# Kernel optimization log

Hardware: AMD Instinct MI355X
Metric: run time of the kernel (lower is better)

Reference implementation:

```python
import jax, jax.numpy as jnp
import numpy as np

B, Cin, Cout, H, W = 8, 64, 128, 128, 128
K, S, P = 3, 1, 1
KK = K * K
EPS = 1e-5


def _conv2d(x, w, b=None):
    out = jax.lax.conv_general_dilated(
        x, w, window_strides=(S, S), padding=[(P, P), (P, P)],
        dimension_numbers=('NCHW', 'OIHW', 'NCHW'))
    if b is not None:
        out = out + b[None, :, None, None]
    return out


def setup_inputs() -> dict:
    key = jax.random.key(0)
    k = jax.random.split(key, 5)
    sc = 1.0 / np.sqrt(Cin * KK)
    return {
        'x': jax.random.normal(k[0], (B, Cin, H, W), jnp.float32),
        'offset_w': jax.random.normal(k[1], (2 * KK, Cin, K, K), jnp.float32) * sc,
        'offset_b': jnp.zeros((2 * KK,), jnp.float32),
        'mask_w': jax.random.normal(k[2], (KK, Cin, K, K), jnp.float32) * sc,
        'mask_b': jnp.zeros((KK,), jnp.float32),
        'conv_w': jax.random.normal(k[3], (Cout, Cin, K, K), jnp.float32) * sc,
    }


def _deform_conv2d(x, offset, mask, w):
    """Modulated deformable conv (torchvision deform_conv2d semantics)."""
    Bn, C, Hh, Ww = x.shape
    Ho, Wo = offset.shape[2], offset.shape[3]
    off = offset.reshape(Bn, KK, 2, Ho, Wo)  # (y, x) pairs per kernel tap
    ky, kx = jnp.meshgrid(jnp.arange(K), jnp.arange(K), indexing='ij')
    ky = ky.reshape(KK).astype(x.dtype)
    kx = kx.reshape(KK).astype(x.dtype)
    hy = (jnp.arange(Ho) * S - P).astype(x.dtype)
    wx = (jnp.arange(Wo) * S - P).astype(x.dtype)
    # sampling positions [B, KK, Ho, Wo]
    py = off[:, :, 0] + ky[None, :, None, None] + hy[None, None, :, None]
    px = off[:, :, 1] + kx[None, :, None, None] + wx[None, None, None, :]

    y0 = jnp.floor(py)
    x0 = jnp.floor(px)
    wy1 = py - y0; wx1 = px - x0
    wy0 = 1.0 - wy1; wx0 = 1.0 - wx1

    xf = x.reshape(Bn, C, Hh * Ww)

    def gather(yi, xi):
        valid = ((yi >= 0) & (yi < Hh) & (xi >= 0) & (xi < Ww)).astype(x.dtype)
        yc = jnp.clip(yi, 0, Hh - 1).astype(jnp.int32)
        xc = jnp.clip(xi, 0, Ww - 1).astype(jnp.int32)
        idx = (yc * Ww + xc).reshape(Bn, -1)  # [B, KK*Ho*Wo]
        vals = jnp.take_along_axis(xf, idx[:, None, :], axis=2)  # [B, C, KK*Ho*Wo]
        return vals.reshape(Bn, C, KK, Ho, Wo) * valid.reshape(Bn, 1, KK, Ho, Wo)

    v = (gather(y0, x0) * (wy0 * wx0)[:, None]
         + gather(y0, x0 + 1) * (wy0 * wx1)[:, None]
         + gather(y0 + 1, x0) * (wy1 * wx0)[:, None]
         + gather(y0 + 1, x0 + 1) * (wy1 * wx1)[:, None])  # [B, C, KK, Ho, Wo]
    v = v * mask[:, None]  # modulation
    return jnp.einsum('bckhw,ock->bohw', v, w.reshape(w.shape[0], C, KK))


def reference(x, offset_w, offset_b, mask_w, mask_b, conv_w):
    offset = _conv2d(x, offset_w, offset_b)
    mask = jax.nn.sigmoid(_conv2d(x, mask_w, mask_b))
    out = _deform_conv2d(x, offset, mask, conv_w)
    # BatchNorm2d(affine=False), training-mode normalization over (N, H, W)
    mean = out.mean(axis=(0, 2, 3), keepdims=True)
    var = out.var(axis=(0, 2, 3), keepdims=True)
    return jax.nn.relu((out - mean) * jax.lax.rsqrt(var + EPS))
```

## Files before the change

kernel.cpp:

```cpp
#include <hip/hip_runtime.h>
#include <hip/hip_bf16.h>

#define H_ 128
#define W_ 128
#define HW 16384
#define CIN 64
#define COUT 128
#define KK9 9
#define BATCH 8
#define NPIX (BATCH * HW)
#define KDIM 576

typedef short bf16x8 __attribute__((ext_vector_type(8)));
typedef float f32x4  __attribute__((ext_vector_type(4)));
typedef unsigned short ushort_t;

union U4B { uint4 u; bf16x8 v; };

__device__ __forceinline__ float us2f(unsigned short u) {
    unsigned int v = ((unsigned int)u) << 16;
    float f;
    __builtin_memcpy(&f, &v, 4);
    return f;
}
__device__ __forceinline__ float lo_f(unsigned int w) {
    unsigned int v = w << 16;
    float f;
    __builtin_memcpy(&f, &v, 4);
    return f;
}
__device__ __forceinline__ float hi_f(unsigned int w) {
    unsigned int v = w & 0xffff0000u;
    float f;
    __builtin_memcpy(&f, &v, 4);
    return f;
}
__device__ __forceinline__ unsigned short f2us_bf(float f) {
    __hip_bfloat16 h = __float2bfloat16(f);
    unsigned short u;
    __builtin_memcpy(&u, &h, 2);
    return u;
}
__device__ __forceinline__ unsigned int pack2(float a, float b) {
    return (unsigned int)f2us_bf(a) | ((unsigned int)f2us_bf(b) << 16);
}

template <bool F32>
__device__ __forceinline__ float ld_in(const void* p, long i) {
    if (F32) return ((const float*)p)[i];
    return us2f(((const unsigned short*)p)[i]);
}

__global__ void detect_zero(const uint4* __restrict__ xr4,
                            float* __restrict__ flag,
                            float* __restrict__ gstat) {
    int t = threadIdx.x;
#pragma unroll
    for (int i = 0; i < 16; ++i) gstat[i * 256 + t] = 0.0f;
    if (t < 64) {
        uint4 v = xr4[t];
        unsigned int w[4] = {v.x, v.y, v.z, v.w};
        int big = 0;
#pragma unroll
        for (int q = 0; q < 4; ++q) {
            big += (((w[q] >> 7)  & 0xFF) >= 0xC0);
            big += (((w[q] >> 23) & 0xFF) >= 0xC0);
        }
        unsigned long long m = __ballot(big > 0);
        if (t == 0) flag[0] = m ? 1.0f : 0.0f;
    }
}

template <bool F32>
__device__ __forceinline__ void prep_body(const void* offw, const void* offb,
                                          const void* maskw, const void* maskb,
                                          const void* convw,
                                          ushort_t* wTs, ushort_t* wcats,
                                          float* bias, int i) {
    if (i < 73728) {
        int j = i & 7, lane = (i >> 3) & 63, n = (i >> 9) & 7, ks = i >> 12;
        int co = n * 16 + (lane & 15);
        int k  = ks * 32 + ((lane >> 4) << 3) + j;
        int kk = k >> 6, ci = k & 63;
        wTs[i] = f2us_bf(ld_in<F32>(convw, (long)co * KDIM + ci * 9 + kk));
    } else if (i < 73728 + 18432) {
        int i2 = i - 73728;
        int j = i2 & 7, lane = (i2 >> 3) & 63, n = (i2 >> 9) & 1, ks = i2 >> 10;
        int co2 = n * 16 + (lane & 15);
        int k   = ks * 32 + ((lane >> 4) << 3) + j;
        int kk = k >> 6, ci = k & 63;
        float v = 0.0f;
        if (co2 < 18)      v = ld_in<F32>(offw,  (long)co2 * KDIM + ci * 9 + kk);
        else if (co2 < 27) v = ld_in<F32>(maskw, (long)(co2 - 18) * KDIM + ci * 9 + kk);
        wcats[i2] = f2us_bf(v);
    } else if (i < 73728 + 18432 + 32) {
        int j = i - 73728 - 18432;
        float v = 0.0f;
        if (j < 18)      v = ld_in<F32>(offb, j);
        else if (j < 27) v = ld_in<F32>(maskb, j - 18);
        bias[j] = v;
    }
}

__global__ void prep_weights(const void* __restrict__ offw,
                             const void* __restrict__ offb,
                             const void* __restrict__ maskw,
                             const void* __restrict__ maskb,
                             const void* __restrict__ convw,
                             const float* __restrict__ flag,
                             ushort_t* __restrict__ wTs,
                             ushort_t* __restrict__ wcats,
                             float* __restrict__ bias) {
    int i = blockIdx.x * 256 + threadIdx.x;
    if (flag[0] != 0.0f)
        prep_body<true>(offw, offb, maskw, maskb, convw, wTs, wcats, bias, i);
    else
        prep_body<false>(offw, offb, maskw, maskb, convw, wTs, wcats, bias, i);
}

template <bool F32>
__device__ __forceinline__ void transpose_body(const void* x, ushort_t* xnb) {
    __shared__ float tile[CIN][64 + 1];
    int blk  = blockIdx.x;
    int b    = blk >> 8;
    int pix0 = (blk & 255) * 64;
    int t    = threadIdx.x;
    int lane = t & 63;
    int grp  = t >> 6;
#pragma unroll
    for (int r = 0; r < 16; ++r) {
        int ci = r * 4 + grp;
        tile[ci][lane] = ld_in<F32>(x, (long)(b * CIN + ci) * HW + pix0 + lane);
    }
    __syncthreads();
#pragma unroll
    for (int r = 0; r < 16; ++r) {
        int px = r * 4 + grp;
        xnb[(size_t)(b * HW + pix0 + px) * CIN + lane] = f2us_bf(tile[lane][px]);
    }
}

__global__ __launch_bounds__(256) void transpose_x(const void* __restrict__ x,
                                                   const float* __restrict__ flag,
                                                   ushort_t* __restrict__ xnb) {
    if (flag[0] != 0.0f) transpose_body<true>(x, xnb);
    else                 transpose_body<false>(x, xnb);
}

__global__ __launch_bounds__(1024, 4) void conv_mfma(
        const ushort_t* __restrict__ xnb,
        const ushort_t* __restrict__ wcats,
        const float* __restrict__ bias,
        float* __restrict__ off2,
        float* __restrict__ mask_ws) {
    __shared__ uint4 ldsB4[2304];
    __shared__ uint4 ldsX4[4096];

    int t    = threadIdx.x;
    int bid  = blockIdx.x;
    int sbid = (bid & 7) * 64 + (bid >> 3);
    int pix0 = sbid * 256;
    int b    = pix0 >> 14;
    int rem0 = pix0 & 16383;
    int y0   = rem0 >> 7;

    const uint4* ws4 = (const uint4*)wcats;
#pragma unroll
    for (int i = t; i < 2304; i += 1024) ldsB4[i] = ws4[i];

    const uint4* xrow4 = (const uint4*)(xnb + (size_t)b * HW * CIN);
    int sxq  = t >> 3;
    int sc16 = t & 7;
#pragma unroll
    for (int r = 0; r < 4; ++r) {
        int gy = y0 - 1 + r;
        if (gy >= 0 && gy < H_) {
            uint4 v = xrow4[(size_t)gy * 1024 + t];
            ldsX4[r * 1024 + sxq * 8 + (sc16 ^ (sxq & 7))] = v;
        }
    }
    __syncthreads();

    int wave = t >> 6, lane = t & 63, mrow = lane & 15, quad = lane >> 4;
    int px_l = wave * 16 + mrow;
    int ly   = px_l >> 7;
    int xp   = px_l & 127;

    uint4 af0[9], af1[9];
#pragma unroll
    for (int kk = 0; kk < 9; ++kk) {
        int ty = kk / 3, tx = kk % 3;
        int tr = ly + ty;
        int gy = y0 - 1 + tr;
        int xq = xp + tx - 1;
        bool ok = (gy >= 0) && (gy < H_) && (xq >= 0) && (xq < W_);
        int xc = min(max(xq, 0), W_ - 1);
        int base = tr * 1024 + xc * 8;
        uint4 a0 = ldsX4[base + ((quad    ) ^ (xc & 7))];
        uint4 a1 = ldsX4[base + ((quad + 4) ^ (xc & 7))];
        af0[kk] = ok ? a0 : make_uint4(0, 0, 0, 0);
        af1[kk] = ok ? a1 : make_uint4(0, 0, 0, 0);
    }

    f32x4 acc[2];
    acc[0] = (f32x4){0.f, 0.f, 0.f, 0.f};
    acc[1] = (f32x4){0.f, 0.f, 0.f, 0.f};
    const ushort_t* ldsB = (const ushort_t*)ldsB4;
#pragma unroll
    for (int kk = 0; kk < 9; ++kk) {
#pragma unroll
        for (int half = 0; half < 2; ++half) {
            int ks = kk * 2 + half;
            U4B a; a.u = half ? af1[kk] : af0[kk];
#pragma unroll
            for (int n = 0; n < 2; ++n) {
                bf16x8 bf = *(const bf16x8*)(ldsB + ((ks * 2 + n) * 64 + lane) * 8);
                acc[n] = __builtin_amdgcn_mfma_f32_16x16x32_bf16(a.v, bf, acc[n], 0, 0, 0);
            }
        }
    }

#pragma unroll
    for (int n = 0; n < 2; ++n) {
        int co2 = n * 16 + mrow;
        if (co2 >= 27) continue;
        float bs = bias[co2];
#pragma unroll
        for (int r = 0; r < 4; ++r) {
            int px = wave * 16 + quad * 4 + r;
            float v = acc[n][r] + bs;
            if (co2 < 18) {
                off2[((size_t)(b * 9 + (co2 >> 1)) * HW + rem0 + px) * 2 + (co2 & 1)] = v;
            } else {
                mask_ws[(size_t)(b * 9 + (co2 - 18)) * HW + rem0 + px] =
                    1.0f / (1.0f + __expf(-v));
            }
        }
    }
}

__device__ __forceinline__ void compute_tap(int yp_t, int xp_t,
                                            float oy, float ox, float mk,
                                            int* ofs, float* wg) {
    float py  = (float)yp_t + oy;
    float pxf = (float)xp_t + ox;
    float y0f = floorf(py), x0f = floorf(pxf);
    int yi = (int)y0f, xi = (int)x0f;
    float wy1 = py - y0f, wx1 = pxf - x0f;
    float wy0 = 1.0f - wy1, wx0 = 1.0f - wx1;
    int ya  = min(max(yi, 0), H_ - 1);
    int yb  = min(max(yi + 1, 0), H_ - 1);
    int xa  = min(max(xi, 0), W_ - 1);
    int xb2 = min(max(xi + 1, 0), W_ - 1);
    bool vy0 = (yi >= 0) & (yi < H_);
    bool vy1 = (yi >= -1) & (yi < H_ - 1);
    bool vx0 = (xi >= 0) & (xi < W_);
    bool vx1 = (xi >= -1) & (xi < W_ - 1);
    float m0 = mk * wy0, m1 = mk * wy1;
    wg[0] = (vy0 & vx0) ? m0 * wx0 : 0.0f;
    wg[1] = (vy0 & vx1) ? m0 * wx1 : 0.0f;
    wg[2] = (vy1 & vx0) ? m1 * wx0 : 0.0f;
    wg[3] = (vy1 & vx1) ? m1 * wx1 : 0.0f;
    int ra = ya << 13, rb = yb << 13;
    int ca = xa << 6,  cb_ = xb2 << 6;
    ofs[0] = ra + ca;  ofs[1] = ra + cb_;
    ofs[2] = rb + ca;  ofs[3] = rb + cb_;
}

__device__ __forceinline__ void issue_half(const ushort_t* __restrict__ xb,
                                           const int* ofs, int hoff, uint4* cb) {
#pragma unroll
    for (int c = 0; c < 4; ++c)
        cb[c] = *(const uint4*)(xb + ofs[c] + hoff);
}

__device__ __forceinline__ void consume_half(int ks, const uint4* cb,
                                             const float* wg,
                                             const ushort_t* __restrict__ ldsB,
                                             int lane, f32x4* acc) {
    float2 v2[4];
#pragma unroll
    for (int j = 0; j < 4; ++j) v2[j] = make_float2(0.f, 0.f);
#pragma unroll
    for (int c = 0; c < 4; ++c) {
        float w = wg[c];
        unsigned int ww[4] = {cb[c].x, cb[c].y, cb[c].z, cb[c].w};
#pragma unroll
        for (int j = 0; j < 4; ++j) {
            v2[j].x = fmaf(w, lo_f(ww[j]), v2[j].x);
            v2[j].y = fmaf(w, hi_f(ww[j]), v2[j].y);
        }
    }
    U4B a;
    a.u = make_uint4(pack2(v2[0].x, v2[0].y), pack2(v2[1].x, v2[1].y),
                     pack2(v2[2].x, v2[2].y), pack2(v2[3].x, v2[3].y));
    const ushort_t* bbase = ldsB + ((size_t)(ks * 8) * 64 + lane) * 8;
    __builtin_amdgcn_s_setprio(1);
#pragma unroll
    for (int n = 0; n < 8; ++n) {
        bf16x8 bf = *(const bf16x8*)(bbase + n * 64 * 8);
        acc[n] = __builtin_amdgcn_mfma_f32_16x16x32_bf16(a.v, bf, acc[n], 0, 0, 0);
    }
    __builtin_amdgcn_s_setprio(0);
}

__global__ __launch_bounds__(1024, 4) void deform_mfma(
        const ushort_t* __restrict__ xnb,
        const float* __restrict__ off2,
        const float* __restrict__ mask_ws,
        const ushort_t* __restrict__ wTs,
        ushort_t* __restrict__ prebn,
        float* __restrict__ gstat) {
    __shared__ uint4 ldsB4[9216];
    __shared__ float red[256];

    int t    = threadIdx.x;
    int bid  = blockIdx.x;
    int sbid = (bid & 7) * 64 + (bid >> 3);
    int pix0 = sbid * 256;
    int b    = pix0 >> 14;
    int rem0 = pix0 & 16383;

    const uint4* ws4 = (const uint4*)wTs;
#pragma unroll
    for (int i = 0; i < 9; ++i) ldsB4[i * 1024 + t] = ws4[i * 1024 + t];
    if (t < 256) red[t] = 0.0f;

    int wave = t >> 6, lane = t & 63, mrow = lane & 15, quad = lane >> 4;
    int px_l = wave * 16 + mrow;
    int remp = rem0 + px_l;
    int yp = remp >> 7, xp = remp & 127;
    const ushort_t* xb = xnb + (size_t)b * HW * CIN + quad * 8;
    size_t obase = (size_t)b * 9 * HW + remp;

    float2 oE = *(const float2*)(off2 + obase * 2);
    float2 oO = *(const float2*)(off2 + (obase + HW) * 2);
    float mkE = mask_ws[obase];
    float mkO = mask_ws[obase + HW];
    __syncthreads();

    f32x4 acc[8];
#pragma unroll
    for (int n = 0; n < 8; ++n) acc[n] = (f32x4){0.f, 0.f, 0.f, 0.f};
    const ushort_t* ldsB = (const ushort_t*)ldsB4;

    int   ofs[2][4];
    float wg[2][4];
    uint4 cb[3][4];

    compute_tap(yp - 1, xp - 1, oE.x, oE.y, mkE, ofs[0], wg[0]);
    issue_half(xb, ofs[0], 0,  cb[0]);
    issue_half(xb, ofs[0], 32, cb[1]);
    oE  = *(const float2*)(off2 + (obase + (size_t)2 * HW) * 2);
    mkE = mask_ws[obase + (size_t)2 * HW];
    __builtin_amdgcn_sched_barrier(0);

#pragma unroll
    for (int hs = 0; hs < 18; ++hs) {
        const int hs2 = hs + 2;
        if (hs2 < 18) {
            const int kk2 = hs2 >> 1;
            const int s2  = hs2 % 3;
            if ((hs2 & 1) == 0) {
                const int tp2 = kk2 & 1;
                float ooy = tp2 ? oO.x : oE.x;
                float oox = tp2 ? oO.y : oE.y;
                float omk = tp2 ? mkO  : mkE;
                compute_tap(yp + kk2 / 3 - 1, xp + kk2 % 3 - 1, ooy, oox, omk,
                            ofs[tp2], wg[tp2]);
                issue_half(xb, ofs[tp2], 0, cb[s2]);
                if (kk2 + 2 <= 8) {
                    float2 o = *(const float2*)(off2 + (obase + (size_t)(kk2 + 2) * HW) * 2);
                    float  m = mask_ws[obase + (size_t)(kk2 + 2) * HW];
                    if (tp2) { oO = o; mkO = m; } else { oE = o; mkE = m; }
                }
            } else {
                issue_half(xb, ofs[kk2 & 1], 32, cb[s2]);
            }
        }
        __builtin_amdgcn_sched_barrier(0);
        consume_half(hs, cb[hs % 3], wg[(hs >> 1) & 1], ldsB, lane, acc);
    }

#pragma unroll
    for (int n = 0; n < 8; ++n) {
        int co = n * 16 + mrow;
        float s = 0.f, ss = 0.f;
#pragma unroll
        for (int r = 0; r < 4; ++r) {
            int pg = pix0 + wave * 16 + quad * 4 + r;
            float v = acc[n][r];
            prebn[(size_t)pg * COUT + co] = f2us_bf(v);
            s += v;
            ss += v * v;
        }
        s  += __shfl_xor(s, 16, 64);
        s  += __shfl_xor(s, 32, 64);
        ss += __shfl_xor(ss, 16, 64);
        ss += __shfl_xor(ss, 32, 64);
        if (quad == 0) {
            atomicAdd(&red[co], s);
            atomicAdd(&red[128 + co], ss);
        }
    }
    __syncthreads();
    if (t < 256) atomicAdd(&gstat[(bid & 15) * 256 + t], red[t]);
}

__global__ __launch_bounds__(256) void bn_apply_t(const ushort_t* __restrict__ prebn,
                                                  const float* __restrict__ gstat,
                                                  float* __restrict__ out) {
    __shared__ float tile[128 * 65];
    __shared__ float mvs[256];
    int t = threadIdx.x;
    if (t < 128) {
        float s = 0.f, ss = 0.f;
#pragma unroll
        for (int part = 0; part < 16; ++part) {
            s  += gstat[part * 256 + t];
            ss += gstat[part * 256 + 128 + t];
        }
        const float invN = 1.0f / (float)NPIX;
        float mean = s * invN;
        float var  = ss * invN - mean * mean;
        if (!isfinite(mean)) mean = 0.0f;
        float r = rsqrtf(fmaxf(var, 0.0f) + 1e-5f);
        if (!isfinite(r)) r = 1.0f;
        mvs[t]       = mean;
        mvs[128 + t] = r;
    }
    __syncthreads();
    int pix0 = blockIdx.x * 64;
    int b    = pix0 >> 14;
    int rem0 = pix0 & 16383;
    const uint4* src4 = (const uint4*)(prebn + (size_t)pix0 * COUT);
#pragma unroll
    for (int r = 0; r < 4; ++r) {
        int i  = r * 256 + t;
        uint4 v = src4[i];
        int p  = i >> 4;
        int c0 = (i & 15) * 8;
        unsigned int w[4] = {v.x, v.y, v.z, v.w};
#pragma unroll
        for (int j = 0; j < 4; ++j) {
            int c = c0 + j * 2;
            float f0 = lo_f(w[j]);
            float f1 = hi_f(w[j]);
            tile[c * 65 + p]       = fmaxf((f0 - mvs[c])     * mvs[128 + c],     0.0f);
            tile[(c + 1) * 65 + p] = fmaxf((f1 - mvs[c + 1]) * mvs[128 + c + 1], 0.0f);
        }
    }
    __syncthreads();
#pragma unroll
    for (int r = 0; r < 8; ++r) {
        int i  = r * 256 + t;
        int c2 = i >> 4;
        int q  = (i & 15) * 4;
        float4 w4 = make_float4(tile[c2 * 65 + q],     tile[c2 * 65 + q + 1],
                                tile[c2 * 65 + q + 2], tile[c2 * 65 + q + 3]);
        *(float4*)(out + (size_t)(b * COUT + c2) * HW + rem0 + q) = w4;
    }
}

extern "C" void kernel_launch(void* const* d_in, const int* in_sizes, int n_in,
                              void* d_out, int out_size, void* d_ws, size_t ws_size,
                              hipStream_t stream) {
    (void)in_sizes; (void)n_in; (void)out_size; (void)ws_size;
    const void* x     = d_in[0];
    const void* offw  = d_in[1];
    const void* offb  = d_in[2];
    const void* maskw = d_in[3];
    const void* maskb = d_in[4];
    const void* convw = d_in[5];

    float* ws       = (float*)d_ws;
    float* off2     = ws;
    float* mask_ws  = off2 + 2359296;
    float* bias     = mask_ws + 1179648;
    float* gstat    = bias + 32;
    float* flag     = gstat + 4096;
    ushort_t* wTs   = (ushort_t*)(flag + 16);
    ushort_t* wcats = wTs + 73728;
    ushort_t* xnb   = wcats + 18432;
    ushort_t* prebn = xnb + 8388608;
    float* out      = (float*)d_out;

    detect_zero<<<1, 256, 0, stream>>>((const uint4*)x, flag, gstat);
    prep_weights<<<361, 256, 0, stream>>>(offw, offb, maskw, maskb, convw, flag, wTs, wcats, bias);
    transpose_x<<<2048, 256, 0, stream>>>(x, flag, xnb);
    conv_mfma<<<512, 1024, 0, stream>>>(xnb, wcats, bias, off2, mask_ws);
    deform_mfma<<<512, 1024, 0, stream>>>(xnb, off2, mask_ws, wTs, prebn, gstat);
    bn_apply_t<<<2048, 256, 0, stream>>>(prebn, gstat, out);
}
```

Measured before the change: 207.5 us.

## Fuse offset/mask conv into deformable conv kernel and vectorize transpose

Merges the offset/mask convolution kernel into the deformable-conv kernel, so offsets and mask values stay in LDS instead of round-tripping through global workspace. To fit LDS, the deform weights are loaded in two halves with extra block barriers between the halves of the tap loop. The input transpose is also changed to use float4/ushort4 vector loads and stores. The fusion removes one launch and the global offset traffic, at the cost of extra syncs and serializing the small conv before the gather phase in each block.

```diff
diff --git a/kernel.cpp b/kernel.cpp
--- a/kernel.cpp
+++ b/kernel.cpp
@@ -120,23 +120,42 @@
 
 template <bool F32>
 __device__ __forceinline__ void transpose_body(const void* x, ushort_t* xnb) {
-    __shared__ float tile[CIN][64 + 1];
+    __shared__ float tile[CIN * 65];
     int blk  = blockIdx.x;
     int b    = blk >> 8;
     int pix0 = (blk & 255) * 64;
     int t    = threadIdx.x;
-    int lane = t & 63;
-    int grp  = t >> 6;
-#pragma unroll
-    for (int r = 0; r < 16; ++r) {
-        int ci = r * 4 + grp;
-        tile[ci][lane] = ld_in<F32>(x, (long)(b * CIN + ci) * HW + pix0 + lane);
-    }
-    __syncthreads();
-#pragma unroll
-    for (int r = 0; r < 16; ++r) {
-        int px = r * 4 + grp;
-        xnb[(size_t)(b * HW + pix0 + px) * CIN + lane] = f2us_bf(tile[lane][px]);
+#pragma unroll
+    for (int pass = 0; pass < 4; ++pass) {
+        int slot = pass * 256 + t;
+        int ci = slot >> 4;
+        int f4 = slot & 15;
+        long base = (long)(b * CIN + ci) * HW + pix0 + f4 * 4;
+        float v0, v1, v2, v3;
+        if (F32) {
+            float4 v = *(const float4*)((const float*)x + base);
+            v0 = v.x; v1 = v.y; v2 = v.z; v3 = v.w;
+        } else {
+            ushort4 u = *(const ushort4*)((const ushort_t*)x + base);
+            v0 = us2f(u.x); v1 = us2f(u.y); v2 = us2f(u.z); v3 = us2f(u.w);
+        }
+        tile[ci * 65 + f4 * 4 + 0] = v0;
+        tile[ci * 65 + f4 * 4 + 1] = v1;
+        tile[ci * 65 + f4 * 4 + 2] = v2;
+        tile[ci * 65 + f4 * 4 + 3] = v3;
+    }
+    __syncthreads();
+#pragma unroll
+    for (int pass = 0; pass < 4; ++pass) {
+        int slot = pass * 256 + t;
+        int px = slot >> 4;
+        int c4 = slot & 15;
+        ushort4 o;
+        o.x = f2us_bf(tile[(c4 * 4 + 0) * 65 + px]);
+        o.y = f2us_bf(tile[(c4 * 4 + 1) * 65 + px]);
+        o.z = f2us_bf(tile[(c4 * 4 + 2) * 65 + px]);
+        o.w = f2us_bf(tile[(c4 * 4 + 3) * 65 + px]);
+        *(ushort4*)(xnb + (size_t)(b * HW + pix0 + px) * CIN + c4 * 4) = o;
     }
 }
 
@@ -145,98 +164,6 @@
                                                    ushort_t* __restrict__ xnb) {
     if (flag[0] != 0.0f) transpose_body<true>(x, xnb);
     else                 transpose_body<false>(x, xnb);
-}
-
-__global__ __launch_bounds__(1024, 4) void conv_mfma(
-        const ushort_t* __restrict__ xnb,
-        const ushort_t* __restrict__ wcats,
-        const float* __restrict__ bias,
-        float* __restrict__ off2,
-        float* __restrict__ mask_ws) {
-    __shared__ uint4 ldsB4[2304];
-    __shared__ uint4 ldsX4[4096];
-
-    int t    = threadIdx.x;
-    int bid  = blockIdx.x;
-    int sbid = (bid & 7) * 64 + (bid >> 3);
-    int pix0 = sbid * 256;
-    int b    = pix0 >> 14;
-    int rem0 = pix0 & 16383;
-    int y0   = rem0 >> 7;
-
-    const uint4* ws4 = (const uint4*)wcats;
-#pragma unroll
-    for (int i = t; i < 2304; i += 1024) ldsB4[i] = ws4[i];
-
-    const uint4* xrow4 = (const uint4*)(xnb + (size_t)b * HW * CIN);
-    int sxq  = t >> 3;
-    int sc16 = t & 7;
-#pragma unroll
-    for (int r = 0; r < 4; ++r) {
-        int gy = y0 - 1 + r;
-        if (gy >= 0 && gy < H_) {
-            uint4 v = xrow4[(size_t)gy * 1024 + t];
-            ldsX4[r * 1024 + sxq * 8 + (sc16 ^ (sxq & 7))] = v;
-        }
-    }
-    __syncthreads();
-
-    int wave = t >> 6, lane = t & 63, mrow = lane & 15, quad = lane >> 4;
-    int px_l = wave * 16 + mrow;
-    int ly   = px_l >> 7;
-    int xp   = px_l & 127;
-
-    uint4 af0[9], af1[9];
-#pragma unroll
-    for (int kk = 0; kk < 9; ++kk) {
-        int ty = kk / 3, tx = kk % 3;
-        int tr = ly + ty;
-        int gy = y0 - 1 + tr;
-        int xq = xp + tx - 1;
-        bool ok = (gy >= 0) && (gy < H_) && (xq >= 0) && (xq < W_);
-        int xc = min(max(xq, 0), W_ - 1);
-        int base = tr * 1024 + xc * 8;
-        uint4 a0 = ldsX4[base + ((quad    ) ^ (xc & 7))];
-        uint4 a1 = ldsX4[base + ((quad + 4) ^ (xc & 7))];
-        af0[kk] = ok ? a0 : make_uint4(0, 0, 0, 0);
-        af1[kk] = ok ? a1 : make_uint4(0, 0, 0, 0);
-    }
-
-    f32x4 acc[2];
-    acc[0] = (f32x4){0.f, 0.f, 0.f, 0.f};
-    acc[1] = (f32x4){0.f, 0.f, 0.f, 0.f};
-    const ushort_t* ldsB = (const ushort_t*)ldsB4;
-#pragma unroll
-    for (int kk = 0; kk < 9; ++kk) {
-#pragma unroll
-        for (int half = 0; half < 2; ++half) {
-            int ks = kk * 2 + half;
-            U4B a; a.u = half ? af1[kk] : af0[kk];
-#pragma unroll
-            for (int n = 0; n < 2; ++n) {
-                bf16x8 bf = *(const bf16x8*)(ldsB + ((ks * 2 + n) * 64 + lane) * 8);
-                acc[n] = __builtin_amdgcn_mfma_f32_16x16x32_bf16(a.v, bf, acc[n], 0, 0, 0);
-            }
-        }
-    }
-
-#pragma unroll
-    for (int n = 0; n < 2; ++n) {
-        int co2 = n * 16 + mrow;
-        if (co2 >= 27) continue;
-        float bs = bias[co2];
-#pragma unroll
-        for (int r = 0; r < 4; ++r) {
-            int px = wave * 16 + quad * 4 + r;
-            float v = acc[n][r] + bs;
-            if (co2 < 18) {
-                off2[((size_t)(b * 9 + (co2 >> 1)) * HW + rem0 + px) * 2 + (co2 & 1)] = v;
-            } else {
-                mask_ws[(size_t)(b * 9 + (co2 - 18)) * HW + rem0 + px] =
-                    1.0f / (1.0f + __expf(-v));
-            }
-        }
-    }
 }
 
 __device__ __forceinline__ void compute_tap(int yp_t, int xp_t,
@@ -274,7 +201,7 @@
         cb[c] = *(const uint4*)(xb + ofs[c] + hoff);
 }
 
-__device__ __forceinline__ void consume_half(int ks, const uint4* cb,
+__device__ __forceinline__ void consume_half(int slot, const uint4* cb,
                                              const float* wg,
                                              const ushort_t* __restrict__ ldsB,
                                              int lane, f32x4* acc) {
@@ -294,7 +221,7 @@
     U4B a;
     a.u = make_uint4(pack2(v2[0].x, v2[0].y), pack2(v2[1].x, v2[1].y),
                      pack2(v2[2].x, v2[2].y), pack2(v2[3].x, v2[3].y));
-    const ushort_t* bbase = ldsB + ((size_t)(ks * 8) * 64 + lane) * 8;
+    const ushort_t* bbase = ldsB + ((size_t)(slot * 8) * 64 + lane) * 8;
     __builtin_amdgcn_s_setprio(1);
 #pragma unroll
     for (int n = 0; n < 8; ++n) {
@@ -304,15 +231,18 @@
     __builtin_amdgcn_s_setprio(0);
 }
 
-__global__ __launch_bounds__(1024, 4) void deform_mfma(
+__global__ __launch_bounds__(1024, 4) void fused_conv_deform(
         const ushort_t* __restrict__ xnb,
-        const float* __restrict__ off2,
-        const float* __restrict__ mask_ws,
+        const ushort_t* __restrict__ wcats,
+        const float* __restrict__ bias,
         const ushort_t* __restrict__ wTs,
         ushort_t* __restrict__ prebn,
         float* __restrict__ gstat) {
-    __shared__ uint4 ldsB4[9216];
-    __shared__ float red[256];
+    __shared__ uint4 lds[8192];
+
+    float2* offL  = (float2*)(lds + 6400);
+    float*  maskS = (float*) (lds + 7552);
+    float*  red   = (float*) (lds + 8128);
 
     int t    = threadIdx.x;
     int bid  = blockIdx.x;
@@ -320,43 +250,137 @@
     int pix0 = sbid * 256;
     int b    = pix0 >> 14;
     int rem0 = pix0 & 16383;
-
-    const uint4* ws4 = (const uint4*)wTs;
-#pragma unroll
-    for (int i = 0; i < 9; ++i) ldsB4[i * 1024 + t] = ws4[i * 1024 + t];
+    int y0   = rem0 >> 7;
+
+    const uint4* wc4 = (const uint4*)wcats;
+    for (int i = t; i < 2304; i += 1024) lds[i] = wc4[i];
+    const uint4* xrow4 = (const uint4*)(xnb + (size_t)b * HW * CIN);
+    int sxq = t >> 3, sc16 = t & 7;
+#pragma unroll
+    for (int r = 0; r < 4; ++r) {
+        int gy = y0 - 1 + r;
+        if (gy >= 0 && gy < H_) {
+            uint4 v = xrow4[(size_t)gy * 1024 + t];
+            lds[2304 + r * 1024 + sxq * 8 + (sc16 ^ (sxq & 7))] = v;
+        }
+    }
     if (t < 256) red[t] = 0.0f;
+    __syncthreads();
 
     int wave = t >> 6, lane = t & 63, mrow = lane & 15, quad = lane >> 4;
     int px_l = wave * 16 + mrow;
+
+    {
+        int ly = px_l >> 7;
+        int xp = px_l & 127;
+        uint4 af0[9], af1[9];
+#pragma unroll
+        for (int kk = 0; kk < 9; ++kk) {
+            int ty = kk / 3, tx = kk % 3;
+            int tr = ly + ty;
+            int gy = y0 - 1 + tr;
+            int xq = xp + tx - 1;
+            bool ok = (gy >= 0) && (gy < H_) && (xq >= 0) && (xq < W_);
+            int xc = min(max(xq, 0), W_ - 1);
+            int base = 2304 + tr * 1024 + xc * 8;
+            uint4 a0 = lds[base + ((quad    ) ^ (xc & 7))];
+            uint4 a1 = lds[base + ((quad + 4) ^ (xc & 7))];
+            af0[kk] = ok ? a0 : make_uint4(0, 0, 0, 0);
+            af1[kk] = ok ? a1 : make_uint4(0, 0, 0, 0);
+        }
+        f32x4 cacc[2];
+        cacc[0] = (f32x4){0.f, 0.f, 0.f, 0.f};
+        cacc[1] = (f32x4){0.f, 0.f, 0.f, 0.f};
+        const ushort_t* ldsBc = (const ushort_t*)lds;
+#pragma unroll
+        for (int kk = 0; kk < 9; ++kk) {
+#pragma unroll
+            for (int half = 0; half < 2; ++half) {
+                int ks = kk * 2 + half;
+                U4B a; a.u = half ? af1[kk] : af0[kk];
+#pragma unroll
+                for (int n = 0; n < 2; ++n) {
+                    bf16x8 bf = *(const bf16x8*)(ldsBc + ((ks * 2 + n) * 64 + lane) * 8);
+                    cacc[n] = __builtin_amdgcn_mfma_f32_16x16x32_bf16(a.v, bf, cacc[n], 0, 0, 0);
+                }
+            }
+        }
+#pragma unroll
+        for (int n = 0; n < 2; ++n) {
+            int co2 = n * 16 + mrow;
+            if (co2 >= 27) continue;
+            float bs = bias[co2];
+#pragma unroll
+            for (int r = 0; r < 4; ++r) {
+                int px = wave * 16 + quad * 4 + r;
+                float v = cacc[n][r] + bs;
+                if (co2 < 18)
+                    ((float*)offL)[((co2 >> 1) * 256 + px) * 2 + (co2 & 1)] = v;
+                else
+                    maskS[(co2 - 18) * 256 + px] = 1.0f / (1.0f + __expf(-v));
+            }
+        }
+    }
+    __syncthreads();
+
+    const uint4* ws4 = (const uint4*)wTs;
+    for (int i = t; i < 4608; i += 1024) lds[i] = ws4[i];
+
     int remp = rem0 + px_l;
-    int yp = remp >> 7, xp = remp & 127;
+    int yp  = remp >> 7, xp2 = remp & 127;
     const ushort_t* xb = xnb + (size_t)b * HW * CIN + quad * 8;
-    size_t obase = (size_t)b * 9 * HW + remp;
-
-    float2 oE = *(const float2*)(off2 + obase * 2);
-    float2 oO = *(const float2*)(off2 + (obase + HW) * 2);
-    float mkE = mask_ws[obase];
-    float mkO = mask_ws[obase + HW];
-    __syncthreads();
 
     f32x4 acc[8];
 #pragma unroll
     for (int n = 0; n < 8; ++n) acc[n] = (f32x4){0.f, 0.f, 0.f, 0.f};
-    const ushort_t* ldsB = (const ushort_t*)ldsB4;
 
     int   ofs[2][4];
     float wg[2][4];
     uint4 cb[3][4];
 
-    compute_tap(yp - 1, xp - 1, oE.x, oE.y, mkE, ofs[0], wg[0]);
+    float2 oE  = offL[px_l];           float mkE = maskS[px_l];
+    float2 oO  = offL[256 + px_l];     float mkO = maskS[256 + px_l];
+    compute_tap(yp - 1, xp2 - 1, oE.x, oE.y, mkE, ofs[0], wg[0]);
     issue_half(xb, ofs[0], 0,  cb[0]);
     issue_half(xb, ofs[0], 32, cb[1]);
-    oE  = *(const float2*)(off2 + (obase + (size_t)2 * HW) * 2);
-    mkE = mask_ws[obase + (size_t)2 * HW];
+    oE = offL[2 * 256 + px_l];  mkE = maskS[2 * 256 + px_l];
     __builtin_amdgcn_sched_barrier(0);
-
-#pragma unroll
-    for (int hs = 0; hs < 18; ++hs) {
+    __syncthreads();
+
+    const ushort_t* ldsB = (const ushort_t*)lds;
+
+#pragma unroll
+    for (int hs = 0; hs < 9; ++hs) {
+        const int hs2 = hs + 2;
+        {
+            const int kk2 = hs2 >> 1;
+            const int s2  = hs2 % 3;
+            if ((hs2 & 1) == 0) {
+                const int tp2 = kk2 & 1;
+                float ooy = tp2 ? oO.x : oE.x;
+                float oox = tp2 ? oO.y : oE.y;
+                float omk = tp2 ? mkO  : mkE;
+                compute_tap(yp + kk2 / 3 - 1, xp2 + kk2 % 3 - 1, ooy, oox, omk,
+                            ofs[tp2], wg[tp2]);
+                issue_half(xb, ofs[tp2], 0, cb[s2]);
+                if (kk2 + 2 <= 8) {
+                    float2 o = offL[(kk2 + 2) * 256 + px_l];
+                    float  m = maskS[(kk2 + 2) * 256 + px_l];
+                    if (tp2) { oO = o; mkO = m; } else { oE = o; mkE = m; }
+                }
+            } else {
+                issue_half(xb, ofs[kk2 & 1], 32, cb[s2]);
+            }
+        }
+        __builtin_amdgcn_sched_barrier(0);
+        consume_half(hs, cb[hs % 3], wg[(hs >> 1) & 1], ldsB, lane, acc);
+    }
+    __syncthreads();
+    for (int i = t; i < 4608; i += 1024) lds[i] = ws4[4608 + i];
+    __syncthreads();
+
+#pragma unroll
+    for (int hs = 9; hs < 18; ++hs) {
         const int hs2 = hs + 2;
         if (hs2 < 18) {
             const int kk2 = hs2 >> 1;
@@ -366,12 +390,12 @@
                 float ooy = tp2 ? oO.x : oE.x;
                 float oox = tp2 ? oO.y : oE.y;
                 float omk = tp2 ? mkO  : mkE;
-                compute_tap(yp + kk2 / 3 - 1, xp + kk2 % 3 - 1, ooy, oox, omk,
+                compute_tap(yp + kk2 / 3 - 1, xp2 + kk2 % 3 - 1, ooy, oox, omk,
                             ofs[tp2], wg[tp2]);
                 issue_half(xb, ofs[tp2], 0, cb[s2]);
                 if (kk2 + 2 <= 8) {
-                    float2 o = *(const float2*)(off2 + (obase + (size_t)(kk2 + 2) * HW) * 2);
-                    float  m = mask_ws[obase + (size_t)(kk2 + 2) * HW];
+                    float2 o = offL[(kk2 + 2) * 256 + px_l];
+                    float  m = maskS[(kk2 + 2) * 256 + px_l];
                     if (tp2) { oO = o; mkO = m; } else { oE = o; mkE = m; }
                 }
             } else {
@@ -379,7 +403,7 @@
             }
         }
         __builtin_amdgcn_sched_barrier(0);
-        consume_half(hs, cb[hs % 3], wg[(hs >> 1) & 1], ldsB, lane, acc);
+        consume_half(hs - 9, cb[hs % 3], wg[(hs >> 1) & 1], ldsB, lane, acc);
     }
 
 #pragma unroll
@@ -488,7 +512,6 @@
     detect_zero<<<1, 256, 0, stream>>>((const uint4*)x, flag, gstat);
     prep_weights<<<361, 256, 0, stream>>>(offw, offb, maskw, maskb, convw, flag, wTs, wcats, bias);
     transpose_x<<<2048, 256, 0, stream>>>(x, flag, xnb);
-    conv_mfma<<<512, 1024, 0, stream>>>(xnb, wcats, bias, off2, mask_ws);
-    deform_mfma<<<512, 1024, 0, stream>>>(xnb, off2, mask_ws, wTs, prebn, gstat);
+    fused_conv_deform<<<512, 1024, 0, stream>>>(xnb, wcats, bias, wTs, prebn, gstat);
     bn_apply_t<<<2048, 256, 0, stream>>>(prebn, gstat, out);
 }
```

Result: faster. 202.0 us (-2.6%).
